# Performance work log

Measured on AMD Instinct MI355X. Metric: run time of the kernel, lower is better.

## Reference

```python
import jax, jax.numpy as jnp
import numpy as np

S = 30.0
M = 0.4
EPS = 1e-07


def setup_inputs() -> dict:
    key = jax.random.key(0)
    k1, k2, k3 = jax.random.split(key, 3)
    B, D, C = 1024, 512, 50000
    x = jax.random.normal(k1, (B, D), dtype=jnp.float32)
    labels = jax.random.randint(k2, (B,), 0, C, dtype=jnp.int64)
    W = jax.random.normal(k3, (C, D), dtype=jnp.float32) * 0.02
    return {"x": x, "labels": labels, "W": W}


def reference(x, labels, W):
    # NOTE: original torch code's weight-normalization loop is a no-op
    # (rebinds a local), so W is used unnormalized. Only x is normalized.
    xn = x / jnp.maximum(jnp.linalg.norm(x, axis=1, keepdims=True), 1e-12)
    cos_theta = xn @ W.T  # [B, C]

    B = x.shape[0]
    rows = jnp.arange(B)
    target = cos_theta[rows, labels]  # [B]
    target = jnp.clip(target, -1.0 + EPS, 1.0 - EPS)
    numerator = S * jnp.cos(jnp.arccos(target) + M)  # [B]

    # sum of exp(s * cos) over all classes except the true one
    exp_all = jnp.exp(S * cos_theta)  # [B, C]
    excl_sum = jnp.sum(exp_all, axis=1) - exp_all[rows, labels]  # [B]

    denominator = jnp.exp(numerator) + excl_sum
    loss = numerator - jnp.log(denominator)
    return (cos_theta, -jnp.mean(loss))
```

## Files before the change

kernel.cpp:

```cpp
#include <hip/hip_runtime.h>
#include <hip/hip_bf16.h>
#include <math.h>


#define DD 512
#define TM 128
#define TN 128
#define TK 32

typedef __attribute__((ext_vector_type(8))) short short8;
typedef __attribute__((ext_vector_type(4))) float f32x4;

__global__ __launch_bounds__(256) void arc_normalize_bf16(const float* __restrict__ x,
                                                          __hip_bfloat16* __restrict__ xn,
                                                          float* __restrict__ sumexp,
                                                          int B) {
    int r = blockIdx.x;
    int tid = threadIdx.x;
    const float* xr = x + (size_t)r * DD;
    float v0 = xr[tid];
    float v1 = xr[tid + 256];
    float ss = v0 * v0 + v1 * v1;
    #pragma unroll
    for (int off = 32; off > 0; off >>= 1) ss += __shfl_down(ss, off, 64);
    __shared__ float wsum[4];
    if ((tid & 63) == 0) wsum[tid >> 6] = ss;
    __syncthreads();
    float tot = wsum[0] + wsum[1] + wsum[2] + wsum[3];
    float inv = 1.0f / fmaxf(sqrtf(tot), 1e-12f);
    xn[(size_t)r * DD + tid] = __float2bfloat16(v0 * inv);
    xn[(size_t)r * DD + tid + 256] = __float2bfloat16(v1 * inv);
    if (tid == 0) sumexp[r] = 0.0f;
}

__global__ __launch_bounds__(256) void arc_cvt_w(const float* __restrict__ W,
                                                 __hip_bfloat16* __restrict__ Wb,
                                                 long n) {
    long i = ((long)blockIdx.x * 256 + threadIdx.x) * 8;
    if (i + 8 <= n) {
        f32x4 a = __builtin_nontemporal_load((const f32x4*)(W + i));
        f32x4 b = __builtin_nontemporal_load((const f32x4*)(W + i + 4));
        union { __hip_bfloat16 h[8]; short8 v; } pk;
        pk.h[0] = __float2bfloat16(a.x); pk.h[1] = __float2bfloat16(a.y);
        pk.h[2] = __float2bfloat16(a.z); pk.h[3] = __float2bfloat16(a.w);
        pk.h[4] = __float2bfloat16(b.x); pk.h[5] = __float2bfloat16(b.y);
        pk.h[6] = __float2bfloat16(b.z); pk.h[7] = __float2bfloat16(b.w);
        *(short8*)(Wb + i) = pk.v;
    } else if (i < n) {
        for (long j = i; j < n; j++) Wb[j] = __float2bfloat16(W[j]);
    }
}

__global__ __launch_bounds__(256) void arc_gemm_mfma(const __hip_bfloat16* __restrict__ A,
                                                     const __hip_bfloat16* __restrict__ Wb,
                                                     float* __restrict__ out,
                                                     float* __restrict__ sumexp,
                                                     int C) {
    __shared__ __hip_bfloat16 Als[TM * TK];
    __shared__ __hip_bfloat16 Bls[TN * TK];

    const int tid = threadIdx.x;
    const int lane = tid & 63;
    const int wave = tid >> 6;
    const int quad = lane >> 4;
    const int l16 = lane & 15;
    const int wm = (wave >> 1) * 64;
    const int wn = (wave & 1) * 64;

    const int nwg = gridDim.x * gridDim.y;
    const int flat = blockIdx.x + gridDim.x * blockIdx.y;
    const int xcd = flat & 7;
    const int pos = flat >> 3;
    const int q = nwg >> 3;
    const int r8 = nwg & 7;
    const int wg = (xcd < r8 ? xcd * (q + 1) : r8 * (q + 1) + (xcd - r8) * q) + pos;
    const int m0 = (wg % gridDim.x) * TM;
    const int n0 = (wg / gridDim.x) * TN;

    f32x4 acc[4][4];
    #pragma unroll
    for (int i = 0; i < 4; i++)
        #pragma unroll
        for (int j = 0; j < 4; j++) acc[i][j] = (f32x4){0.f, 0.f, 0.f, 0.f};

    const int rowA = tid >> 2, ch = tid & 3;
    const __hip_bfloat16* gA0 = A + (size_t)(m0 + rowA) * DD + ch * 8;
    const __hip_bfloat16* gA1 = gA0 + (size_t)64 * DD;
    int nr0 = n0 + rowA;      if (nr0 >= C) nr0 = C - 1;
    int nr1 = n0 + 64 + rowA; if (nr1 >= C) nr1 = C - 1;
    const __hip_bfloat16* gB0 = Wb + (size_t)nr0 * DD + ch * 8;
    const __hip_bfloat16* gB1 = Wb + (size_t)nr1 * DD + ch * 8;

    char* ldsA0 = (char*)Als + (tid & ~63) * 16;
    char* ldsA1 = ldsA0 + 4096;
    char* ldsB0 = (char*)Bls + (tid & ~63) * 16;
    char* ldsB1 = ldsB0 + 4096;

    for (int k0 = 0; k0 < DD; k0 += TK) {
        __builtin_amdgcn_global_load_lds(
            (const __attribute__((address_space(1))) void*)(gA0 + k0),
            (__attribute__((address_space(3))) void*)ldsA0, 16, 0, 0);
        __builtin_amdgcn_global_load_lds(
            (const __attribute__((address_space(1))) void*)(gA1 + k0),
            (__attribute__((address_space(3))) void*)ldsA1, 16, 0, 0);
        __builtin_amdgcn_global_load_lds(
            (const __attribute__((address_space(1))) void*)(gB0 + k0),
            (__attribute__((address_space(3))) void*)ldsB0, 16, 0, 0);
        __builtin_amdgcn_global_load_lds(
            (const __attribute__((address_space(1))) void*)(gB1 + k0),
            (__attribute__((address_space(3))) void*)ldsB1, 16, 0, 0);
        __syncthreads();

        short8 af[4], bfr[4];
        #pragma unroll
        for (int mi = 0; mi < 4; mi++)
            af[mi] = *(const short8*)((const char*)Als + ((wm + mi * 16 + l16) * TK + quad * 8) * 2);
        #pragma unroll
        for (int ni = 0; ni < 4; ni++)
            bfr[ni] = *(const short8*)((const char*)Bls + ((wn + ni * 16 + l16) * TK + quad * 8) * 2);

        #pragma unroll
        for (int mi = 0; mi < 4; mi++)
            #pragma unroll
            for (int ni = 0; ni < 4; ni++)
                acc[mi][ni] = __builtin_amdgcn_mfma_f32_16x16x32_bf16(
                    af[mi], bfr[ni], acc[mi][ni], 0, 0, 0);
        __syncthreads();
    }

    const bool full = (n0 + TN <= C);
    #pragma unroll
    for (int mi = 0; mi < 4; mi++) {
        float se[4] = {0.f, 0.f, 0.f, 0.f};
        #pragma unroll
        for (int ni = 0; ni < 4; ni++) {
            int n = n0 + wn + ni * 16 + l16;
            f32x4 v = acc[mi][ni];
            if (full || n < C) {
                size_t base = (size_t)(m0 + wm + mi * 16 + quad * 4) * C + n;
                #pragma unroll
                for (int r = 0; r < 4; r++) {
                    __builtin_nontemporal_store(v[r], &out[base + (size_t)r * C]);
                    se[r] += expf(30.0f * v[r]);
                }
            }
        }
        #pragma unroll
        for (int off = 1; off < 16; off <<= 1) {
            #pragma unroll
            for (int r = 0; r < 4; r++) se[r] += __shfl_xor(se[r], off, 64);
        }
        if (l16 == 0) {
            int mbase = m0 + wm + mi * 16 + quad * 4;
            #pragma unroll
            for (int r = 0; r < 4; r++) atomicAdd(&sumexp[mbase + r], se[r]);
        }
    }
}

#define BM 128
#define BN 128
#define BK 16
__global__ __launch_bounds__(256) void arc_normalize_f32(const float* __restrict__ x,
                                                         float* __restrict__ xn,
                                                         float* __restrict__ sumexp,
                                                         int B) {
    int r = blockIdx.x;
    int tid = threadIdx.x;
    const float* xr = x + (size_t)r * DD;
    float v0 = xr[tid];
    float v1 = xr[tid + 256];
    float ss = v0 * v0 + v1 * v1;
    #pragma unroll
    for (int off = 32; off > 0; off >>= 1) ss += __shfl_down(ss, off, 64);
    __shared__ float wsum[4];
    if ((tid & 63) == 0) wsum[tid >> 6] = ss;
    __syncthreads();
    float tot = wsum[0] + wsum[1] + wsum[2] + wsum[3];
    float inv = 1.0f / fmaxf(sqrtf(tot), 1e-12f);
    xn[(size_t)r * DD + tid] = v0 * inv;
    xn[(size_t)r * DD + tid + 256] = v1 * inv;
    if (tid == 0) sumexp[r] = 0.0f;
}

__global__ __launch_bounds__(256) void arc_gemm_f32(const float* __restrict__ A,
                                                    const float* __restrict__ Wm,
                                                    float* __restrict__ out,
                                                    float* __restrict__ sumexp,
                                                    int B, int C) {
    __shared__ float As[BK][BM];
    __shared__ float Bs[BK][BN];
    const int m0 = blockIdx.x * BM;
    const int n0 = blockIdx.y * BN;
    const int tid = threadIdx.x;
    const int tx = tid & 15;
    const int ty = tid >> 4;
    float acc[8][8];
    #pragma unroll
    for (int i = 0; i < 8; i++)
        #pragma unroll
        for (int j = 0; j < 8; j++) acc[i][j] = 0.0f;
    for (int k0 = 0; k0 < DD; k0 += BK) {
        #pragma unroll
        for (int l = 0; l < 2; l++) {
            int f = tid + l * 256;
            int row = f >> 2, kc = f & 3;
            float4 v = *(const float4*)(A + (size_t)(m0 + row) * DD + k0 + kc * 4);
            As[kc * 4 + 0][row] = v.x; As[kc * 4 + 1][row] = v.y;
            As[kc * 4 + 2][row] = v.z; As[kc * 4 + 3][row] = v.w;
        }
        #pragma unroll
        for (int l = 0; l < 2; l++) {
            int f = tid + l * 256;
            int row = f >> 2, kc = f & 3;
            int n = n0 + row;
            float4 v = make_float4(0.f, 0.f, 0.f, 0.f);
            if (n < C) v = *(const float4*)(Wm + (size_t)n * DD + k0 + kc * 4);
            Bs[kc * 4 + 0][row] = v.x; Bs[kc * 4 + 1][row] = v.y;
            Bs[kc * 4 + 2][row] = v.z; Bs[kc * 4 + 3][row] = v.w;
        }
        __syncthreads();
        #pragma unroll
        for (int k = 0; k < BK; k++) {
            float4 a0 = *(const float4*)&As[k][ty * 8];
            float4 a1 = *(const float4*)&As[k][ty * 8 + 4];
            float4 b0 = *(const float4*)&Bs[k][tx * 8];
            float4 b1 = *(const float4*)&Bs[k][tx * 8 + 4];
            float a[8] = {a0.x, a0.y, a0.z, a0.w, a1.x, a1.y, a1.z, a1.w};
            float b[8] = {b0.x, b0.y, b0.z, b0.w, b1.x, b1.y, b1.z, b1.w};
            #pragma unroll
            for (int i = 0; i < 8; i++)
                #pragma unroll
                for (int j = 0; j < 8; j++) acc[i][j] = fmaf(a[i], b[j], acc[i][j]);
        }
        __syncthreads();
    }
    const bool full = (n0 + BN <= C);
    #pragma unroll
    for (int i = 0; i < 8; i++) {
        int m = m0 + ty * 8 + i;
        float* orow = out + (size_t)m * C + n0 + tx * 8;
        float s = 0.0f;
        if (full) {
            *(float4*)orow = make_float4(acc[i][0], acc[i][1], acc[i][2], acc[i][3]);
            *(float4*)(orow + 4) = make_float4(acc[i][4], acc[i][5], acc[i][6], acc[i][7]);
            #pragma unroll
            for (int j = 0; j < 8; j++) s += expf(30.0f * acc[i][j]);
        } else {
            #pragma unroll
            for (int j = 0; j < 8; j++) {
                int n = n0 + tx * 8 + j;
                if (n < C) { orow[j] = acc[i][j]; s += expf(30.0f * acc[i][j]); }
            }
        }
        #pragma unroll
        for (int off = 1; off < 16; off <<= 1) s += __shfl_xor(s, off, 64);
        if (tx == 0) atomicAdd(&sumexp[m], s);
    }
}

__global__ __launch_bounds__(1024) void arc_finalize(const float* __restrict__ cosm,
                                                     const int* __restrict__ labels,
                                                     const float* __restrict__ sumexp,
                                                     float* __restrict__ out_loss,
                                                     int B, int C) {
    int r = threadIdx.x;
    float loss = 0.0f;
    if (r < B) {
        int lab = labels[r];
        float t_raw = cosm[(size_t)r * C + lab];
        float se = sumexp[r];
        float t = fminf(fmaxf(t_raw, -1.0f + 1e-7f), 1.0f - 1e-7f);
        const float cosM = 0.9210609940028851f;
        const float sinM = 0.3894183423086505f;
        float num = 30.0f * (t * cosM - sqrtf(fmaxf(1.0f - t * t, 0.0f)) * sinM);
        float excl = se - expf(30.0f * t_raw);
        float denom = expf(num) + excl;
        loss = num - logf(denom);
    }
    __shared__ float red[1024];
    red[threadIdx.x] = loss;
    __syncthreads();
    for (int s = 512; s > 0; s >>= 1) {
        if (threadIdx.x < s) red[threadIdx.x] += red[threadIdx.x + s];
        __syncthreads();
    }
    if (threadIdx.x == 0) out_loss[0] = -red[0] / (float)B;
}

extern "C" void kernel_launch(void* const* d_in, const int* in_sizes, int n_in,
                              void* d_out, int out_size, void* d_ws, size_t ws_size,
                              hipStream_t stream) {
    const float* x = (const float*)d_in[0];
    const int* labels = (const int*)d_in[1];
    const float* Wm = (const float*)d_in[2];
    int B = in_sizes[1];
    int C = in_sizes[2] / DD;
    float* out = (float*)d_out;

    size_t need = 4096 + (size_t)B * DD * 2 + (size_t)C * DD * 2 + 256;
    if (ws_size >= need) {
        float* sumexp = (float*)d_ws;
        __hip_bfloat16* xnb = (__hip_bfloat16*)((char*)d_ws + 4096);
        __hip_bfloat16* Wb = xnb + (size_t)B * DD;

        arc_normalize_bf16<<<B, 256, 0, stream>>>(x, xnb, sumexp, B);
        long wn = (long)C * DD;
        long nblk = (wn / 8 + 255) / 256;
        arc_cvt_w<<<(int)nblk, 256, 0, stream>>>(Wm, Wb, wn);
        dim3 grid(B / TM, (C + TN - 1) / TN);
        arc_gemm_mfma<<<grid, 256, 0, stream>>>(xnb, Wb, out, sumexp, C);
        arc_finalize<<<1, 1024, 0, stream>>>(out, labels, sumexp, out + (size_t)B * C, B, C);
    } else {
        float* xn = (float*)d_ws;
        float* sumexp = xn + (size_t)B * DD;
        arc_normalize_f32<<<B, 256, 0, stream>>>(x, xn, sumexp, B);
        dim3 grid(B / BM, (C + BN - 1) / BN);
        arc_gemm_f32<<<grid, 256, 0, stream>>>(xn, Wm, out, sumexp, B, C);
        arc_finalize<<<1, 1024, 0, stream>>>(out, labels, sumexp, out + (size_t)B * C, B, C);
    }
}
```

Baseline: 387.2 us.

## Fuse fp32-to-bf16 weight conversion into GEMM with double-buffered LDS pipeline

Removes the separate kernel that converted W to bf16. The GEMM now loads fp32 W tiles straight into registers, converts them, and writes them to a double-buffered LDS tile while the MFMAs on the current buffer run. A tiles are also prefetched into the alternate buffer. This saves a kernel launch and the write and re-read of the bf16 copy of W, in exchange for reading fp32 W once per M-block (8 blocks, so twice the bytes of the bf16 reads) and doing conversion work inside the GEMM loop.

```diff
diff --git a/kernel.cpp b/kernel.cpp
--- a/kernel.cpp
+++ b/kernel.cpp
@@ -7,6 +7,7 @@
 #define TM 128
 #define TN 128
 #define TK 32
+#define NSTEP (DD / TK)
 
 typedef __attribute__((ext_vector_type(8))) short short8;
 typedef __attribute__((ext_vector_type(4))) float f32x4;
@@ -33,31 +34,13 @@
     if (tid == 0) sumexp[r] = 0.0f;
 }
 
-__global__ __launch_bounds__(256) void arc_cvt_w(const float* __restrict__ W,
-                                                 __hip_bfloat16* __restrict__ Wb,
-                                                 long n) {
-    long i = ((long)blockIdx.x * 256 + threadIdx.x) * 8;
-    if (i + 8 <= n) {
-        f32x4 a = __builtin_nontemporal_load((const f32x4*)(W + i));
-        f32x4 b = __builtin_nontemporal_load((const f32x4*)(W + i + 4));
-        union { __hip_bfloat16 h[8]; short8 v; } pk;
-        pk.h[0] = __float2bfloat16(a.x); pk.h[1] = __float2bfloat16(a.y);
-        pk.h[2] = __float2bfloat16(a.z); pk.h[3] = __float2bfloat16(a.w);
-        pk.h[4] = __float2bfloat16(b.x); pk.h[5] = __float2bfloat16(b.y);
-        pk.h[6] = __float2bfloat16(b.z); pk.h[7] = __float2bfloat16(b.w);
-        *(short8*)(Wb + i) = pk.v;
-    } else if (i < n) {
-        for (long j = i; j < n; j++) Wb[j] = __float2bfloat16(W[j]);
-    }
-}
-
-__global__ __launch_bounds__(256) void arc_gemm_mfma(const __hip_bfloat16* __restrict__ A,
-                                                     const __hip_bfloat16* __restrict__ Wb,
-                                                     float* __restrict__ out,
-                                                     float* __restrict__ sumexp,
-                                                     int C) {
-    __shared__ __hip_bfloat16 Als[TM * TK];
-    __shared__ __hip_bfloat16 Bls[TN * TK];
+__global__ __launch_bounds__(256) void arc_gemm_fused(const __hip_bfloat16* __restrict__ A,
+                                                      const float* __restrict__ W,
+                                                      float* __restrict__ out,
+                                                      float* __restrict__ sumexp,
+                                                      int C) {
+    __shared__ __hip_bfloat16 Als[2][TM * TK];
+    __shared__ __hip_bfloat16 Bls[2][TN * TK];
 
     const int tid = threadIdx.x;
     const int lane = tid & 63;
@@ -86,38 +69,73 @@
     const int rowA = tid >> 2, ch = tid & 3;
     const __hip_bfloat16* gA0 = A + (size_t)(m0 + rowA) * DD + ch * 8;
     const __hip_bfloat16* gA1 = gA0 + (size_t)64 * DD;
-    int nr0 = n0 + rowA;      if (nr0 >= C) nr0 = C - 1;
-    int nr1 = n0 + 64 + rowA; if (nr1 >= C) nr1 = C - 1;
-    const __hip_bfloat16* gB0 = Wb + (size_t)nr0 * DD + ch * 8;
-    const __hip_bfloat16* gB1 = Wb + (size_t)nr1 * DD + ch * 8;
-
-    char* ldsA0 = (char*)Als + (tid & ~63) * 16;
-    char* ldsA1 = ldsA0 + 4096;
-    char* ldsB0 = (char*)Bls + (tid & ~63) * 16;
-    char* ldsB1 = ldsB0 + 4096;
-
-    for (int k0 = 0; k0 < DD; k0 += TK) {
-        __builtin_amdgcn_global_load_lds(
-            (const __attribute__((address_space(1))) void*)(gA0 + k0),
-            (__attribute__((address_space(3))) void*)ldsA0, 16, 0, 0);
-        __builtin_amdgcn_global_load_lds(
-            (const __attribute__((address_space(1))) void*)(gA1 + k0),
-            (__attribute__((address_space(3))) void*)ldsA1, 16, 0, 0);
-        __builtin_amdgcn_global_load_lds(
-            (const __attribute__((address_space(1))) void*)(gB0 + k0),
-            (__attribute__((address_space(3))) void*)ldsB0, 16, 0, 0);
-        __builtin_amdgcn_global_load_lds(
-            (const __attribute__((address_space(1))) void*)(gB1 + k0),
-            (__attribute__((address_space(3))) void*)ldsB1, 16, 0, 0);
-        __syncthreads();
+
+    const int rB = tid >> 2;
+    const int kcB = (tid & 3) * 8;
+    int nB0 = n0 + rB;       if (nB0 >= C) nB0 = C - 1;
+    int nB1 = n0 + 64 + rB;  if (nB1 >= C) nB1 = C - 1;
+    const float* gW0 = W + (size_t)nB0 * DD + kcB;
+    const float* gW1 = W + (size_t)nB1 * DD + kcB;
+
+    f32x4 b00, b01, b10, b11;
+
+#define ISSUE_A(t, buf)                                                              \
+    do {                                                                             \
+        char* d0_ = (char*)&Als[(buf)][0] + (tid & ~63) * 16;                        \
+        __builtin_amdgcn_global_load_lds(                                            \
+            (const __attribute__((address_space(1))) void*)(gA0 + (t) * TK),         \
+            (__attribute__((address_space(3))) void*)d0_, 16, 0, 0);                 \
+        __builtin_amdgcn_global_load_lds(                                            \
+            (const __attribute__((address_space(1))) void*)(gA1 + (t) * TK),         \
+            (__attribute__((address_space(3))) void*)(d0_ + 4096), 16, 0, 0);        \
+    } while (0)
+
+#define LOAD_B(t)                                                                    \
+    do {                                                                             \
+        const float* p0_ = gW0 + (t) * TK;                                           \
+        const float* p1_ = gW1 + (t) * TK;                                           \
+        b00 = *(const f32x4*)(p0_);                                                  \
+        b01 = *(const f32x4*)(p0_ + 4);                                              \
+        b10 = *(const f32x4*)(p1_);                                                  \
+        b11 = *(const f32x4*)(p1_ + 4);                                              \
+    } while (0)
+
+#define WRITE_B(buf)                                                                 \
+    do {                                                                             \
+        union { __hip_bfloat16 h[8]; short8 v; } p0_, p1_;                           \
+        p0_.h[0] = __float2bfloat16(b00.x); p0_.h[1] = __float2bfloat16(b00.y);      \
+        p0_.h[2] = __float2bfloat16(b00.z); p0_.h[3] = __float2bfloat16(b00.w);      \
+        p0_.h[4] = __float2bfloat16(b01.x); p0_.h[5] = __float2bfloat16(b01.y);      \
+        p0_.h[6] = __float2bfloat16(b01.z); p0_.h[7] = __float2bfloat16(b01.w);      \
+        p1_.h[0] = __float2bfloat16(b10.x); p1_.h[1] = __float2bfloat16(b10.y);      \
+        p1_.h[2] = __float2bfloat16(b10.z); p1_.h[3] = __float2bfloat16(b10.w);      \
+        p1_.h[4] = __float2bfloat16(b11.x); p1_.h[5] = __float2bfloat16(b11.y);      \
+        p1_.h[6] = __float2bfloat16(b11.z); p1_.h[7] = __float2bfloat16(b11.w);      \
+        *(short8*)((char*)&Bls[(buf)][0] + tid * 16) = p0_.v;                        \
+        *(short8*)((char*)&Bls[(buf)][0] + tid * 16 + 4096) = p1_.v;                 \
+    } while (0)
+
+    ISSUE_A(0, 0);
+    LOAD_B(0);
+    WRITE_B(0);
+    __syncthreads();
+
+    for (int t = 0; t < NSTEP; t++) {
+        const int cur = t & 1, nxt = cur ^ 1;
+        if (t + 1 < NSTEP) {
+            ISSUE_A(t + 1, nxt);
+            LOAD_B(t + 1);
+        }
 
         short8 af[4], bfr[4];
         #pragma unroll
         for (int mi = 0; mi < 4; mi++)
-            af[mi] = *(const short8*)((const char*)Als + ((wm + mi * 16 + l16) * TK + quad * 8) * 2);
+            af[mi] = *(const short8*)((const char*)&Als[cur][0] +
+                                      ((wm + mi * 16 + l16) * TK + quad * 8) * 2);
         #pragma unroll
         for (int ni = 0; ni < 4; ni++)
-            bfr[ni] = *(const short8*)((const char*)Bls + ((wn + ni * 16 + l16) * TK + quad * 8) * 2);
+            bfr[ni] = *(const short8*)((const char*)&Bls[cur][0] +
+                                       ((wn + ni * 16 + l16) * TK + quad * 8) * 2);
 
         #pragma unroll
         for (int mi = 0; mi < 4; mi++)
@@ -125,6 +143,8 @@
             for (int ni = 0; ni < 4; ni++)
                 acc[mi][ni] = __builtin_amdgcn_mfma_f32_16x16x32_bf16(
                     af[mi], bfr[ni], acc[mi][ni], 0, 0, 0);
+
+        if (t + 1 < NSTEP) WRITE_B(nxt);
         __syncthreads();
     }
 
@@ -156,6 +176,9 @@
             for (int r = 0; r < 4; r++) atomicAdd(&sumexp[mbase + r], se[r]);
         }
     }
+#undef ISSUE_A
+#undef LOAD_B
+#undef WRITE_B
 }
 
 #define BM 128
@@ -298,18 +321,14 @@
     int C = in_sizes[2] / DD;
     float* out = (float*)d_out;
 
-    size_t need = 4096 + (size_t)B * DD * 2 + (size_t)C * DD * 2 + 256;
+    size_t need = 4096 + (size_t)B * DD * 2 + 256;
     if (ws_size >= need) {
         float* sumexp = (float*)d_ws;
         __hip_bfloat16* xnb = (__hip_bfloat16*)((char*)d_ws + 4096);
-        __hip_bfloat16* Wb = xnb + (size_t)B * DD;
 
         arc_normalize_bf16<<<B, 256, 0, stream>>>(x, xnb, sumexp, B);
-        long wn = (long)C * DD;
-        long nblk = (wn / 8 + 255) / 256;
-        arc_cvt_w<<<(int)nblk, 256, 0, stream>>>(Wm, Wb, wn);
         dim3 grid(B / TM, (C + TN - 1) / TN);
-        arc_gemm_mfma<<<grid, 256, 0, stream>>>(xnb, Wb, out, sumexp, C);
+        arc_gemm_fused<<<grid, 256, 0, stream>>>(xnb, Wm, out, sumexp, C);
         arc_finalize<<<1, 1024, 0, stream>>>(out, labels, sumexp, out + (size_t)B * C, B, C);
     } else {
         float* xn = (float*)d_ws;
```

Result: slower. 410.7 us (+6.0%).

## Double-buffer LDS tiles in the MFMA GEMM and use plain output stores

Applied to the files above, without the earlier changes.

The GEMM now keeps two LDS buffers for the A and B tiles. It issues the global-to-LDS loads for the next K step right after the barrier, so they overlap the MFMA work on the current step, and this drops one barrier per iteration. The cosine output writes also change from nontemporal stores to ordinary stores. The cost is twice the LDS per workgroup, which may lower occupancy, and a different cache behaviour for the large output write.

```diff
diff --git a/kernel.cpp b/kernel.cpp
--- a/kernel.cpp
+++ b/kernel.cpp
@@ -7,6 +7,7 @@
 #define TM 128
 #define TN 128
 #define TK 32
+#define NSTEP (DD / TK)
 
 typedef __attribute__((ext_vector_type(8))) short short8;
 typedef __attribute__((ext_vector_type(4))) float f32x4;
@@ -56,8 +57,8 @@
                                                      float* __restrict__ out,
                                                      float* __restrict__ sumexp,
                                                      int C) {
-    __shared__ __hip_bfloat16 Als[TM * TK];
-    __shared__ __hip_bfloat16 Bls[TN * TK];
+    __shared__ __hip_bfloat16 Als[2][TM * TK];
+    __shared__ __hip_bfloat16 Bls[2][TN * TK];
 
     const int tid = threadIdx.x;
     const int lane = tid & 63;
@@ -91,33 +92,43 @@
     const __hip_bfloat16* gB0 = Wb + (size_t)nr0 * DD + ch * 8;
     const __hip_bfloat16* gB1 = Wb + (size_t)nr1 * DD + ch * 8;
 
-    char* ldsA0 = (char*)Als + (tid & ~63) * 16;
-    char* ldsA1 = ldsA0 + 4096;
-    char* ldsB0 = (char*)Bls + (tid & ~63) * 16;
-    char* ldsB1 = ldsB0 + 4096;
-
-    for (int k0 = 0; k0 < DD; k0 += TK) {
-        __builtin_amdgcn_global_load_lds(
-            (const __attribute__((address_space(1))) void*)(gA0 + k0),
-            (__attribute__((address_space(3))) void*)ldsA0, 16, 0, 0);
-        __builtin_amdgcn_global_load_lds(
-            (const __attribute__((address_space(1))) void*)(gA1 + k0),
-            (__attribute__((address_space(3))) void*)ldsA1, 16, 0, 0);
-        __builtin_amdgcn_global_load_lds(
-            (const __attribute__((address_space(1))) void*)(gB0 + k0),
-            (__attribute__((address_space(3))) void*)ldsB0, 16, 0, 0);
-        __builtin_amdgcn_global_load_lds(
-            (const __attribute__((address_space(1))) void*)(gB1 + k0),
-            (__attribute__((address_space(3))) void*)ldsB1, 16, 0, 0);
+    const int ldsOff = (tid & ~63) * 16;
+
+#define ISSUE(t, buf)                                                                \
+    do {                                                                             \
+        char* dA_ = (char*)&Als[(buf)][0] + ldsOff;                                  \
+        char* dB_ = (char*)&Bls[(buf)][0] + ldsOff;                                  \
+        __builtin_amdgcn_global_load_lds(                                            \
+            (const __attribute__((address_space(1))) void*)(gA0 + (t) * TK),         \
+            (__attribute__((address_space(3))) void*)dA_, 16, 0, 0);                 \
+        __builtin_amdgcn_global_load_lds(                                            \
+            (const __attribute__((address_space(1))) void*)(gA1 + (t) * TK),         \
+            (__attribute__((address_space(3))) void*)(dA_ + 4096), 16, 0, 0);        \
+        __builtin_amdgcn_global_load_lds(                                            \
+            (const __attribute__((address_space(1))) void*)(gB0 + (t) * TK),         \
+            (__attribute__((address_space(3))) void*)dB_, 16, 0, 0);                 \
+        __builtin_amdgcn_global_load_lds(                                            \
+            (const __attribute__((address_space(1))) void*)(gB1 + (t) * TK),         \
+            (__attribute__((address_space(3))) void*)(dB_ + 4096), 16, 0, 0);        \
+    } while (0)
+
+    ISSUE(0, 0);
+
+    for (int t = 0; t < NSTEP; t++) {
+        const int cur = t & 1, nxt = cur ^ 1;
         __syncthreads();
 
+        if (t + 1 < NSTEP) ISSUE(t + 1, nxt);
+
         short8 af[4], bfr[4];
         #pragma unroll
         for (int mi = 0; mi < 4; mi++)
-            af[mi] = *(const short8*)((const char*)Als + ((wm + mi * 16 + l16) * TK + quad * 8) * 2);
+            af[mi] = *(const short8*)((const char*)&Als[cur][0] +
+                                      ((wm + mi * 16 + l16) * TK + quad * 8) * 2);
         #pragma unroll
         for (int ni = 0; ni < 4; ni++)
-            bfr[ni] = *(const short8*)((const char*)Bls + ((wn + ni * 16 + l16) * TK + quad * 8) * 2);
+            bfr[ni] = *(const short8*)((const char*)&Bls[cur][0] +
+                                       ((wn + ni * 16 + l16) * TK + quad * 8) * 2);
 
         #pragma unroll
         for (int mi = 0; mi < 4; mi++)
@@ -125,8 +136,8 @@
             for (int ni = 0; ni < 4; ni++)
                 acc[mi][ni] = __builtin_amdgcn_mfma_f32_16x16x32_bf16(
                     af[mi], bfr[ni], acc[mi][ni], 0, 0, 0);
-        __syncthreads();
-    }
+    }
+#undef ISSUE
 
     const bool full = (n0 + TN <= C);
     #pragma unroll
@@ -140,7 +151,7 @@
                 size_t base = (size_t)(m0 + wm + mi * 16 + quad * 4) * C + n;
                 #pragma unroll
                 for (int r = 0; r < 4; r++) {
-                    __builtin_nontemporal_store(v[r], &out[base + (size_t)r * C]);
+                    out[base + (size_t)r * C] = v[r];
                     se[r] += expf(30.0f * v[r]);
                 }
             }
```

Measured after the change: 387.4 us. Within noise of the previous version (+0.0%).
